# Kernel tuning notes

Measured on AMD Instinct MI355X. Metric: run time of the kernel, lower is better.

Reference implementation:

```python
import jax, jax.numpy as jnp
import numpy as np

E, N, NB = 250000, 20000, 8
D_EDGE, D_RBF, D_CBF, D_TRI = 128, 16, 16, 64
INV_SQRT_2 = 1.0 / np.sqrt(2.0).astype(np.float32)
INV_SQRT_NB = 1.0 / np.sqrt(float(NB))


def setup_inputs() -> dict:
    key = jax.random.key(0)
    ks = jax.random.split(key, 13)
    def w(k, fi, fo):
        return (jax.random.normal(k, (fi, fo), dtype=jnp.float32) / np.sqrt(fi)).astype(jnp.float32)
    return {
        "m_st": jax.random.normal(ks[0], (E, D_EDGE), dtype=jnp.float32),
        "rbf": jax.random.normal(ks[1], (E, D_RBF), dtype=jnp.float32),
        "cbf": jax.random.normal(ks[2], (E, NB, D_CBF), dtype=jnp.float32),
        "idx_s": jax.random.randint(ks[3], (E,), 0, N),
        "idx_swap": jax.random.randint(ks[4], (E,), 0, E),
        "basis_idx1": jax.random.randint(ks[5], (N, NB), 0, E),
        "W_m_rbf": w(ks[6], D_EDGE, D_EDGE),
        "W_rbf": w(ks[7], D_RBF, D_EDGE),
        "W_m_cbf": w(ks[8], D_EDGE, D_TRI),
        "W_cbf": w(ks[9], D_CBF, D_TRI),
        "W_dir": w(ks[10], D_TRI, D_EDGE),
        "W_st": w(ks[11], D_EDGE, D_EDGE),
        "W_ts": w(ks[12], D_EDGE, D_EDGE),
    }


def reference(m_st, rbf, cbf, idx_s, idx_swap, basis_idx1,
              W_m_rbf, W_rbf, W_m_cbf, W_cbf, W_dir, W_st, W_ts):
    act = jax.nn.silu
    # gather per-edge basis indices: (E, NB) -> (E*NB,)
    b1 = basis_idx1[idx_s].reshape(-1)
    # rbf branch (ScaleFactor == 1.0 at init -> identity)
    m = act(m_st @ W_m_rbf)                     # (E, D_EDGE)
    m = m * (rbf @ W_rbf)                       # (E, D_EDGE)
    # cbf branch
    e, nb, c = cbf.shape
    cbf2 = cbf.reshape(e * nb, c)               # (E*NB, D_CBF)
    m_nb = act(m @ W_m_cbf)                     # (E, D_TRI)
    m_nb = m_nb[b1]                             # gather -> (E*NB, D_TRI)
    m_nb = m_nb * (cbf2 @ W_cbf)                # (E*NB, D_TRI)
    x = m_nb.reshape(e, nb, -1).sum(1) * INV_SQRT_NB  # (E, D_TRI)
    x = act(x @ W_dir)                          # (E, D_EDGE)
    x_st = act(x @ W_st)
    x_ts = act(x @ W_ts)[idx_swap]              # swap-gather
    return (x_st + x_ts) * INV_SQRT_2
```

## Files before the change

kernel.cpp:

```cpp
#include <hip/hip_runtime.h>


#define DEV __device__ __forceinline__

typedef __attribute__((ext_vector_type(8))) short bf16x8;
typedef __attribute__((ext_vector_type(4))) float f32x4;

constexpr int E = 250000;
constexpr float INV_SQRT_2  = 0.70710678118654752f;
constexpr float INV_SQRT_NB = 0.35355339059327373f;

constexpr int PW1 = 0;
constexpr int PW2 = 16384;
constexpr int PW3 = 20480;
constexpr int PWD = 28672;
constexpr int PWS = 36864;
constexpr int PWT = 53248;
constexpr int PWC = 69632;
constexpr int PACK_TOTAL = 72192;

constexpr size_t OFF_T = 1u << 18;
constexpr size_t OFF_Z = OFF_T + (size_t)E * 64 * 2;
constexpr size_t WS_NEED_FAST = OFF_Z + (size_t)E * 128 * 4;

DEV unsigned short f2bf(float f) {
  __bf16 h = (__bf16)f;
  unsigned short u;
  __builtin_memcpy(&u, &h, 2);
  return u;
}
DEV unsigned f2bfpk(float lo, float hi) {
  return (unsigned)f2bf(lo) | ((unsigned)f2bf(hi) << 16);
}
DEV float bf2f(unsigned short h) { return __uint_as_float((unsigned)h << 16); }
DEV float silu_f(float x) { return x / (1.f + __expf(-x)); }

__global__ __launch_bounds__(256) void k0_pack(
    const float* __restrict__ W1, const float* __restrict__ W2,
    const float* __restrict__ W3, const float* __restrict__ Wc,
    const float* __restrict__ Wd, const float* __restrict__ Ws,
    const float* __restrict__ Wt, unsigned short* __restrict__ pack) {
  int idx = blockIdx.x * 256 + threadIdx.x;
  if (idx >= PACK_TOTAL) return;
  float v = 0.f;
  if (idx < PW2)      { int i = idx;       int n = i >> 7, k = i & 127; v = W1[k * 128 + n]; }
  else if (idx < PW3) { int i = idx - PW2; int n = i >> 5, k = i & 31;  v = (k < 16) ? W2[k * 128 + n] : 0.f; }
  else if (idx < PWD) { int i = idx - PW3; int n = i >> 7, k = i & 127; v = W3[k * 64 + n]; }
  else if (idx < PWS) { int i = idx - PWD; int n = i >> 6, k = i & 63;  v = Wd[k * 128 + n]; }
  else if (idx < PWT) { int i = idx - PWS; int n = i >> 7, k = i & 127; v = Ws[k * 128 + n]; }
  else if (idx < PWC) { int i = idx - PWT; int n = i >> 7, k = i & 127; v = Wt[k * 128 + n]; }
  else                { int i = idx - PWC; int n = i / 40, k = i % 40;  v = (k < 16) ? Wc[k * 64 + n] : 0.f; }
  pack[idx] = f2bf(v);
}

__global__ __launch_bounds__(512) void k1_mbranch(
    const float* __restrict__ m_st, const float* __restrict__ rbf,
    const unsigned short* __restrict__ pack, unsigned short* __restrict__ tT) {
  __shared__ __align__(16) unsigned short sA[128 * 136];
  __shared__ __align__(16) unsigned short sR[128 * 40];
  const int tid = threadIdx.x;
  const int e0 = blockIdx.x * 128;

  #pragma unroll
  for (int it = 0; it < 8; ++it) {
    int i = tid + it * 512;
    int row = i >> 5, kh = i & 31;
    int er = min(e0 + row, E - 1);
    const float4 v = *(const float4*)(m_st + (size_t)er * 128 + kh * 4);
    uint2 o;
    o.x = f2bfpk(v.x, v.y); o.y = f2bfpk(v.z, v.w);
    *(uint2*)(sA + row * 136 + kh * 4) = o;
  }
  {
    int row = tid >> 2, kh = tid & 3;
    int er = min(e0 + row, E - 1);
    const float4 v = *(const float4*)(rbf + (size_t)er * 16 + kh * 4);
    uint2 o;
    o.x = f2bfpk(v.x, v.y); o.y = f2bfpk(v.z, v.w);
    *(uint2*)(sR + row * 40 + kh * 4) = o;
    uint2 zz = {0u, 0u};
    *(uint2*)(sR + row * 40 + 16 + kh * 4) = zz;
  }
  __syncthreads();

  const int lane = tid & 63, wv = tid >> 6;
  const int m = lane & 15, q = lane >> 4;
  const int arow = wv * 16 + m;

  const f32x4 zero4 = {0.f, 0.f, 0.f, 0.f};
  f32x4 macc[8], racc[8];
  #pragma unroll
  for (int nt = 0; nt < 8; ++nt) { macc[nt] = zero4; racc[nt] = zero4; }

  {
    bf16x8 a = *(const bf16x8*)(sR + arow * 40 + q * 8);
    #pragma unroll
    for (int nt = 0; nt < 8; ++nt) {
      bf16x8 b = *(const bf16x8*)(pack + PW2 + (nt * 16 + m) * 32 + q * 8);
      racc[nt] = __builtin_amdgcn_mfma_f32_16x16x32_bf16(a, b, racc[nt], 0, 0, 0);
    }
  }
  #pragma unroll
  for (int kk = 0; kk < 4; ++kk) {
    bf16x8 a = *(const bf16x8*)(sA + arow * 136 + kk * 32 + q * 8);
    #pragma unroll
    for (int nt = 0; nt < 8; ++nt) {
      bf16x8 b = *(const bf16x8*)(pack + PW1 + (nt * 16 + m) * 128 + kk * 32 + q * 8);
      macc[nt] = __builtin_amdgcn_mfma_f32_16x16x32_bf16(a, b, macc[nt], 0, 0, 0);
    }
  }
  #pragma unroll
  for (int nt = 0; nt < 8; ++nt)
    #pragma unroll
    for (int r = 0; r < 4; ++r) {
      float v = silu_f(macc[nt][r]) * racc[nt][r];
      sA[(wv * 16 + q * 4 + r) * 136 + nt * 16 + m] = f2bf(v);
    }
  __syncthreads();

  f32x4 tacc[4];
  #pragma unroll
  for (int nt = 0; nt < 4; ++nt) tacc[nt] = zero4;
  #pragma unroll
  for (int kk = 0; kk < 4; ++kk) {
    bf16x8 a = *(const bf16x8*)(sA + arow * 136 + kk * 32 + q * 8);
    #pragma unroll
    for (int nt = 0; nt < 4; ++nt) {
      bf16x8 b = *(const bf16x8*)(pack + PW3 + (nt * 16 + m) * 128 + kk * 32 + q * 8);
      tacc[nt] = __builtin_amdgcn_mfma_f32_16x16x32_bf16(a, b, tacc[nt], 0, 0, 0);
    }
  }
  #pragma unroll
  for (int r = 0; r < 4; ++r) {
    int erow = e0 + wv * 16 + q * 4 + r;
    if (erow < E) {
      uint2 o;
      o.x = f2bfpk(silu_f(tacc[0][r]), silu_f(tacc[1][r]));
      o.y = f2bfpk(silu_f(tacc[2][r]), silu_f(tacc[3][r]));
      *(uint2*)(tT + (size_t)erow * 64 + m * 4) = o;
    }
  }
}

DEV bf16x8 cbf_pack8(const float4& c0, const float4& c1) {
  unsigned u[4];
  u[0] = f2bfpk(c0.x, c0.y);
  u[1] = f2bfpk(c0.z, c0.w);
  u[2] = f2bfpk(c1.x, c1.y);
  u[3] = f2bfpk(c1.z, c1.w);
  bf16x8 r;
  __builtin_memcpy(&r, u, 16);
  return r;
}

DEV void x_issue(const float* __restrict__ cbf, const int* sB,
                 const unsigned short* __restrict__ tT,
                 int wv, int m, int q, int mt, long long rowA, long long rowB,
                 float4& c0, float4& c1, ushort4* tv) {
  if (q < 2) {
    long long row = (m < 8) ? rowA + m : rowB + (m - 8);
    c0 = *(const float4*)(cbf + row * 16 + q * 8);
    c1 = *(const float4*)(cbf + row * 16 + q * 8 + 4);
  }
  const int lrb = wv * 128 + mt * 16 + q * 4;
  #pragma unroll
  for (int r = 0; r < 4; ++r) {
    int brow = sB[lrb + r];
    tv[r] = *(const ushort4*)(tT + (size_t)brow * 64 + m * 4);
  }
}

DEV void x_compute(const bf16x8* bw, unsigned short* sX,
                   int wv, int m, int q, int mt,
                   const float4& c0, const float4& c1,
                   const ushort4& tv0, const ushort4& tv1,
                   const ushort4& tv2, const ushort4& tv3) {
  bf16x8 af = {0, 0, 0, 0, 0, 0, 0, 0};
  if (q < 2) af = cbf_pack8(c0, c1);
  const f32x4 zero4 = {0.f, 0.f, 0.f, 0.f};
  f32x4 p0 = zero4, p1 = zero4, p2 = zero4, p3 = zero4;
  p0 = __builtin_amdgcn_mfma_f32_16x16x32_bf16(af, bw[0], p0, 0, 0, 0);
  p1 = __builtin_amdgcn_mfma_f32_16x16x32_bf16(af, bw[1], p1, 0, 0, 0);
  p2 = __builtin_amdgcn_mfma_f32_16x16x32_bf16(af, bw[2], p2, 0, 0, 0);
  p3 = __builtin_amdgcn_mfma_f32_16x16x32_bf16(af, bw[3], p3, 0, 0, 0);

  float s0 = bf2f(tv0.x) * p0[0] + bf2f(tv1.x) * p0[1] + bf2f(tv2.x) * p0[2] + bf2f(tv3.x) * p0[3];
  float s1 = bf2f(tv0.y) * p1[0] + bf2f(tv1.y) * p1[1] + bf2f(tv2.y) * p1[2] + bf2f(tv3.y) * p1[3];
  float s2 = bf2f(tv0.z) * p2[0] + bf2f(tv1.z) * p2[1] + bf2f(tv2.z) * p2[2] + bf2f(tv3.z) * p2[3];
  float s3 = bf2f(tv0.w) * p3[0] + bf2f(tv1.w) * p3[1] + bf2f(tv2.w) * p3[2] + bf2f(tv3.w) * p3[3];

  s0 += __shfl_xor(s0, 16);
  s1 += __shfl_xor(s1, 16);
  s2 += __shfl_xor(s2, 16);
  s3 += __shfl_xor(s3, 16);

  int lrow = wv * 16 + mt * 2 + (q >> 1);
  if (q == 0 || q == 2) {
    sX[lrow * 72 +  0 + m] = f2bf(s0 * INV_SQRT_NB);
    sX[lrow * 72 + 16 + m] = f2bf(s1 * INV_SQRT_NB);
    sX[lrow * 72 + 32 + m] = f2bf(s2 * INV_SQRT_NB);
    sX[lrow * 72 + 48 + m] = f2bf(s3 * INV_SQRT_NB);
  }
}

DEV void xtile_gather_reduce(
    const float* __restrict__ cbf, const int* sB,
    const unsigned short* __restrict__ tT, const bf16x8* bw,
    unsigned short* sX,
    int wv, int m, int q, long long rowA, long long rowB, int mt) {
  float4 c0, c1;
  ushort4 tv[4];
  x_issue(cbf, sB, tT, wv, m, q, mt, rowA, rowB, c0, c1, tv);
  x_compute(bw, sX, wv, m, q, mt, c0, c1, tv[0], tv[1], tv[2], tv[3]);
}

DEV void ytile(const unsigned short* __restrict__ pack,
               const unsigned short* sX,
               unsigned short* sY, int wv, int m, int q) {
  const int arow = wv * 16 + m;
  const f32x4 zero4 = {0.f, 0.f, 0.f, 0.f};
  f32x4 yacc[8];
  #pragma unroll
  for (int nt = 0; nt < 8; ++nt) yacc[nt] = zero4;
  #pragma unroll
  for (int kk = 0; kk < 2; ++kk) {
    bf16x8 a = *(const bf16x8*)(sX + arow * 72 + kk * 32 + q * 8);
    #pragma unroll
    for (int nt = 0; nt < 8; ++nt) {
      bf16x8 b = *(const bf16x8*)(pack + PWD + (nt * 16 + m) * 64 + kk * 32 + q * 8);
      yacc[nt] = __builtin_amdgcn_mfma_f32_16x16x32_bf16(a, b, yacc[nt], 0, 0, 0);
    }
  }
  #pragma unroll
  for (int nt = 0; nt < 8; ++nt)
    #pragma unroll
    for (int r = 0; r < 4; ++r)
      sY[(wv * 16 + q * 4 + r) * 136 + nt * 16 + m] = f2bf(silu_f(yacc[nt][r]));
}

__global__ __launch_bounds__(512) void k2_fused(
    const float* __restrict__ cbf, const int* __restrict__ idx_s,
    const int* __restrict__ basis_idx1, const unsigned short* __restrict__ pack,
    const unsigned short* __restrict__ tT, float* __restrict__ out,
    float* __restrict__ zbuf) {
  __shared__ __align__(16) unsigned char sU[34816];
  __shared__ __align__(16) unsigned short sX[128 * 72];
  unsigned short* sWc = (unsigned short*)sU;
  int* sB1 = (int*)(sU + 5120);
  unsigned short* sY = (unsigned short*)sU;
  const int tid = threadIdx.x;
  const int e0 = blockIdx.x * 128;

  ((uint2*)sWc)[tid] = ((const uint2*)(pack + PWC))[tid];
  if (tid < 128) ((uint2*)sWc)[512 + tid] = ((const uint2*)(pack + PWC))[512 + tid];
  #pragma unroll
  for (int it = 0; it < 2; ++it) {
    int i = tid + it * 512;
    int e = min(e0 + (i >> 3), E - 1);
    int b = basis_idx1[idx_s[e] * 8 + (i & 7)];
    sB1[i] = min(max(b, 0), E - 1);
  }
  __syncthreads();

  const int lane = tid & 63, wv = tid >> 6;
  const int m = lane & 15, q = lane >> 4;

  bf16x8 bw[4];
  #pragma unroll
  for (int nt = 0; nt < 4; ++nt)
    bw[nt] = *(const bf16x8*)(sWc + (nt * 16 + m) * 40 + q * 8);

  float4 pc0[2], pc1[2];
  ushort4 ptv[2][4];
  {
    int ea = min(e0 + wv * 16, E - 1), eb = min(ea + 1, E - 1);
    x_issue(cbf, sB1, tT, wv, m, q, 0, (long long)ea * 8, (long long)eb * 8,
            pc0[0], pc1[0], ptv[0]);
    ea = min(e0 + wv * 16 + 2, E - 1); eb = min(ea + 1, E - 1);
    x_issue(cbf, sB1, tT, wv, m, q, 1, (long long)ea * 8, (long long)eb * 8,
            pc0[1], pc1[1], ptv[1]);
  }
  #pragma unroll
  for (int mt = 0; mt < 8; ++mt) {
    const int s = mt & 1;
    float4 c0 = pc0[s], c1 = pc1[s];
    ushort4 tv0 = ptv[s][0], tv1 = ptv[s][1], tv2 = ptv[s][2], tv3 = ptv[s][3];
    if (mt + 2 < 8) {
      int ea = min(e0 + wv * 16 + (mt + 2) * 2, E - 1), eb = min(ea + 1, E - 1);
      x_issue(cbf, sB1, tT, wv, m, q, mt + 2, (long long)ea * 8, (long long)eb * 8,
              pc0[s], pc1[s], ptv[s]);
    }
    x_compute(bw, sX, wv, m, q, mt, c0, c1, tv0, tv1, tv2, tv3);
  }
  __syncthreads();

  ytile(pack, sX, sY, wv, m, q);
  __syncthreads();

  const int arow = wv * 16 + m;
  const f32x4 zero4 = {0.f, 0.f, 0.f, 0.f};
  f32x4 acc[8];
  #pragma unroll
  for (int nt = 0; nt < 8; ++nt) acc[nt] = zero4;
  #pragma unroll
  for (int kk = 0; kk < 4; ++kk) {
    bf16x8 a = *(const bf16x8*)(sY + arow * 136 + kk * 32 + q * 8);
    #pragma unroll
    for (int nt = 0; nt < 8; ++nt) {
      bf16x8 b = *(const bf16x8*)(pack + PWS + (nt * 16 + m) * 128 + kk * 32 + q * 8);
      acc[nt] = __builtin_amdgcn_mfma_f32_16x16x32_bf16(a, b, acc[nt], 0, 0, 0);
    }
  }
  #pragma unroll
  for (int nt = 0; nt < 8; ++nt)
    #pragma unroll
    for (int r = 0; r < 4; ++r) {
      int erow = e0 + wv * 16 + q * 4 + r;
      if (erow < E) out[(size_t)erow * 128 + nt * 16 + m] = silu_f(acc[nt][r]);
    }

  if (zbuf) {
    #pragma unroll
    for (int nt = 0; nt < 8; ++nt) acc[nt] = zero4;
    #pragma unroll
    for (int kk = 0; kk < 4; ++kk) {
      bf16x8 a = *(const bf16x8*)(sY + arow * 136 + kk * 32 + q * 8);
      #pragma unroll
      for (int nt = 0; nt < 8; ++nt) {
        bf16x8 b = *(const bf16x8*)(pack + PWT + (nt * 16 + m) * 128 + kk * 32 + q * 8);
        acc[nt] = __builtin_amdgcn_mfma_f32_16x16x32_bf16(a, b, acc[nt], 0, 0, 0);
      }
    }
    #pragma unroll
    for (int nt = 0; nt < 8; ++nt)
      #pragma unroll
      for (int r = 0; r < 4; ++r) {
        int erow = e0 + wv * 16 + q * 4 + r;
        if (erow < E) zbuf[(size_t)erow * 128 + nt * 16 + m] = silu_f(acc[nt][r]);
      }
  }
}

__global__ __launch_bounds__(256) void k3_combine(
    const int* __restrict__ idx_swap, const float* __restrict__ zbuf,
    float* __restrict__ out) {
  int t = blockIdx.x * 256 + threadIdx.x;
  int e = t >> 5, c = t & 31;
  if (e >= E) return;
  int f = idx_swap[e];
  f = min(max(f, 0), E - 1);
  float4 o = ((const float4*)out)[t];
  float4 z = ((const float4*)zbuf)[(size_t)f * 32 + c];
  o.x = (o.x + z.x) * INV_SQRT_2;
  o.y = (o.y + z.y) * INV_SQRT_2;
  o.z = (o.z + z.z) * INV_SQRT_2;
  o.w = (o.w + z.w) * INV_SQRT_2;
  ((float4*)out)[t] = o;
}

__global__ __launch_bounds__(512) void k3_swap(
    const float* __restrict__ cbf, const int* __restrict__ idx_s,
    const int* __restrict__ idx_swap, const int* __restrict__ basis_idx1,
    const unsigned short* __restrict__ pack, const unsigned short* __restrict__ tT,
    float* __restrict__ out) {
  __shared__ __align__(16) unsigned short sWc[64 * 40];
  __shared__ int sSE[128];
  __shared__ int sB3[1024];
  __shared__ __align__(16) unsigned short sX[128 * 72];
  __shared__ __align__(16) unsigned short sY[128 * 136];
  const int tid = threadIdx.x;
  const int e0 = blockIdx.x * 128;

  ((uint2*)sWc)[tid] = ((const uint2*)(pack + PWC))[tid];
  if (tid < 128) {
    ((uint2*)sWc)[512 + tid] = ((const uint2*)(pack + PWC))[512 + tid];
    int f = idx_swap[min(e0 + tid, E - 1)];
    sSE[tid] = min(max(f, 0), E - 1);
  }
  __syncthreads();
  #pragma unroll
  for (int it = 0; it < 2; ++it) {
    int i = tid + it * 512;
    int f = sSE[i >> 3];
    int b = basis_idx1[idx_s[f] * 8 + (i & 7)];
    sB3[i] = min(max(b, 0), E - 1);
  }
  __syncthreads();

  const int lane = tid & 63, wv = tid >> 6;
  const int m = lane & 15, q = lane >> 4;

  bf16x8 bw[4];
  #pragma unroll
  for (int nt = 0; nt < 4; ++nt)
    bw[nt] = *(const bf16x8*)(sWc + (nt * 16 + m) * 40 + q * 8);

  for (int mt = 0; mt < 8; ++mt) {
    int le = wv * 16 + mt * 2;
    long long fa = sSE[le], fb = sSE[le + 1];
    xtile_gather_reduce(cbf, sB3, tT, bw, sX, wv, m, q, fa * 8, fb * 8, mt);
  }
  __syncthreads();

  ytile(pack, sX, sY, wv, m, q);
  __syncthreads();

  const int arow = wv * 16 + m;
  const f32x4 zero4 = {0.f, 0.f, 0.f, 0.f};
  f32x4 acc[8];
  #pragma unroll
  for (int nt = 0; nt < 8; ++nt) acc[nt] = zero4;
  #pragma unroll
  for (int kk = 0; kk < 4; ++kk) {
    bf16x8 a = *(const bf16x8*)(sY + arow * 136 + kk * 32 + q * 8);
    #pragma unroll
    for (int nt = 0; nt < 8; ++nt) {
      bf16x8 b = *(const bf16x8*)(pack + PWT + (nt * 16 + m) * 128 + kk * 32 + q * 8);
      acc[nt] = __builtin_amdgcn_mfma_f32_16x16x32_bf16(a, b, acc[nt], 0, 0, 0);
    }
  }
  #pragma unroll
  for (int nt = 0; nt < 8; ++nt)
    #pragma unroll
    for (int r = 0; r < 4; ++r) {
      int erow = e0 + wv * 16 + q * 4 + r;
      if (erow < E) {
        size_t o = (size_t)erow * 128 + nt * 16 + m;
        out[o] = (out[o] + silu_f(acc[nt][r])) * INV_SQRT_2;
      }
    }
}

extern "C" void kernel_launch(void* const* d_in, const int* in_sizes, int n_in,
                              void* d_out, int out_size, void* d_ws, size_t ws_size,
                              hipStream_t stream) {
  const float* m_st = (const float*)d_in[0];
  const float* rbf  = (const float*)d_in[1];
  const float* cbf  = (const float*)d_in[2];
  const int* idx_s  = (const int*)d_in[3];
  const int* idx_sw = (const int*)d_in[4];
  const int* bidx   = (const int*)d_in[5];
  const float* W1 = (const float*)d_in[6];
  const float* W2 = (const float*)d_in[7];
  const float* W3 = (const float*)d_in[8];
  const float* Wc = (const float*)d_in[9];
  const float* Wd = (const float*)d_in[10];
  const float* Ws = (const float*)d_in[11];
  const float* Wt = (const float*)d_in[12];

  unsigned short* pack = (unsigned short*)d_ws;
  unsigned short* tT   = (unsigned short*)((char*)d_ws + OFF_T);
  float* zbuf = (ws_size >= WS_NEED_FAST) ? (float*)((char*)d_ws + OFF_Z) : nullptr;
  float* out = (float*)d_out;

  const int nb = (E + 127) / 128;
  k0_pack<<<(PACK_TOTAL + 255) / 256, 256, 0, stream>>>(W1, W2, W3, Wc, Wd, Ws, Wt, pack);
  k1_mbranch<<<nb, 512, 0, stream>>>(m_st, rbf, pack, tT);
  k2_fused<<<nb, 512, 0, stream>>>(cbf, idx_s, bidx, pack, tT, out, zbuf);
  if (zbuf) {
    k3_combine<<<(E * 32 + 255) / 256, 256, 0, stream>>>(idx_sw, zbuf, out);
  } else {
    k3_swap<<<nb, 512, 0, stream>>>(cbf, idx_s, idx_sw, bidx, pack, tT, out);
  }
}
```

Before: 639.5 us.

## Split fused cbf gather kernel into gather pass and GEMM pass via workspace

```diff
diff --git a/kernel.cpp b/kernel.cpp
--- a/kernel.cpp
+++ b/kernel.cpp
@@ -22,6 +22,8 @@
 constexpr size_t OFF_T = 1u << 18;
 constexpr size_t OFF_Z = OFF_T + (size_t)E * 64 * 2;
 constexpr size_t WS_NEED_FAST = OFF_Z + (size_t)E * 128 * 4;
+constexpr size_t OFF_X = WS_NEED_FAST;
+constexpr size_t WS_NEED_SPLIT = OFF_X + (size_t)E * 64 * 2;
 
 DEV unsigned short f2bf(float f) {
   __bf16 h = (__bf16)f;
@@ -238,6 +240,149 @@
       sY[(wv * 16 + q * 4 + r) * 136 + nt * 16 + m] = f2bf(silu_f(yacc[nt][r]));
 }
 
+__global__ __launch_bounds__(512) void k2a_gather(
+    const float* __restrict__ cbf, const int* __restrict__ idx_s,
+    const int* __restrict__ basis_idx1, const unsigned short* __restrict__ pack,
+    const unsigned short* __restrict__ tT, unsigned short* __restrict__ xbuf) {
+  __shared__ __align__(16) unsigned short sWc[64 * 40];
+  __shared__ int sB1[1024];
+  const int tid = threadIdx.x;
+  const int e0 = blockIdx.x * 128;
+
+  ((uint2*)sWc)[tid] = ((const uint2*)(pack + PWC))[tid];
+  if (tid < 128) ((uint2*)sWc)[512 + tid] = ((const uint2*)(pack + PWC))[512 + tid];
+  #pragma unroll
+  for (int it = 0; it < 2; ++it) {
+    int i = tid + it * 512;
+    int e = min(e0 + (i >> 3), E - 1);
+    int b = basis_idx1[idx_s[e] * 8 + (i & 7)];
+    sB1[i] = min(max(b, 0), E - 1);
+  }
+  __syncthreads();
+
+  const int lane = tid & 63, wv = tid >> 6;
+  const int m = lane & 15, q = lane >> 4;
+
+  bf16x8 bw[4];
+  #pragma unroll
+  for (int nt = 0; nt < 4; ++nt)
+    bw[nt] = *(const bf16x8*)(sWc + (nt * 16 + m) * 40 + q * 8);
+
+  const f32x4 zero4 = {0.f, 0.f, 0.f, 0.f};
+  #pragma unroll
+  for (int mt = 0; mt < 8; ++mt) {
+    int ea = min(e0 + wv * 16 + mt * 2, E - 1), eb = min(ea + 1, E - 1);
+    bf16x8 af = {0, 0, 0, 0, 0, 0, 0, 0};
+    if (q < 2) {
+      long long row = (long long)((m < 8) ? ea : eb) * 8 + (m & 7);
+      float4 c0 = *(const float4*)(cbf + row * 16 + q * 8);
+      float4 c1 = *(const float4*)(cbf + row * 16 + q * 8 + 4);
+      af = cbf_pack8(c0, c1);
+    }
+    f32x4 p0 = __builtin_amdgcn_mfma_f32_16x16x32_bf16(af, bw[0], zero4, 0, 0, 0);
+    f32x4 p1 = __builtin_amdgcn_mfma_f32_16x16x32_bf16(af, bw[1], zero4, 0, 0, 0);
+    f32x4 p2 = __builtin_amdgcn_mfma_f32_16x16x32_bf16(af, bw[2], zero4, 0, 0, 0);
+    f32x4 p3 = __builtin_amdgcn_mfma_f32_16x16x32_bf16(af, bw[3], zero4, 0, 0, 0);
+
+    const int lrb = wv * 128 + mt * 16 + q * 4;
+    float s0 = 0.f, s1 = 0.f, s2 = 0.f, s3 = 0.f;
+    #pragma unroll
+    for (int r = 0; r < 4; ++r) {
+      int brow = sB1[lrb + r];
+      ushort4 tv = *(const ushort4*)(tT + (size_t)brow * 64 + m * 4);
+      s0 += bf2f(tv.x) * p0[r];
+      s1 += bf2f(tv.y) * p1[r];
+      s2 += bf2f(tv.z) * p2[r];
+      s3 += bf2f(tv.w) * p3[r];
+    }
+    s0 += __shfl_xor(s0, 16);
+    s1 += __shfl_xor(s1, 16);
+    s2 += __shfl_xor(s2, 16);
+    s3 += __shfl_xor(s3, 16);
+
+    if (q == 0 || q == 2) {
+      int erow = e0 + wv * 16 + mt * 2 + (q >> 1);
+      if (erow < E) {
+        ushort4 o;
+        o.x = f2bf(s0 * INV_SQRT_NB);
+        o.y = f2bf(s1 * INV_SQRT_NB);
+        o.z = f2bf(s2 * INV_SQRT_NB);
+        o.w = f2bf(s3 * INV_SQRT_NB);
+        *(ushort4*)(xbuf + (size_t)erow * 64 + m * 4) = o;
+      }
+    }
+  }
+}
+
+__global__ __launch_bounds__(512) void k2b_gemm(
+    const unsigned short* __restrict__ pack, const unsigned short* __restrict__ xbuf,
+    float* __restrict__ out, float* __restrict__ zbuf) {
+  __shared__ __align__(16) unsigned short sX[128 * 72];
+  __shared__ __align__(16) unsigned short sY[128 * 136];
+  const int tid = threadIdx.x;
+  const int e0 = blockIdx.x * 128;
+
+  #pragma unroll
+  for (int it = 0; it < 4; ++it) {
+    int i = tid + it * 512;
+    int row = i >> 4, mm = i & 15;
+    int er = min(e0 + row, E - 1);
+    ushort4 v = *(const ushort4*)(xbuf + (size_t)er * 64 + mm * 4);
+    sX[row * 72 +  0 + mm] = v.x;
+    sX[row * 72 + 16 + mm] = v.y;
+    sX[row * 72 + 32 + mm] = v.z;
+    sX[row * 72 + 48 + mm] = v.w;
+  }
+  __syncthreads();
+
+  const int lane = tid & 63, wv = tid >> 6;
+  const int m = lane & 15, q = lane >> 4;
+
+  ytile(pack, sX, sY, wv, m, q);
+  __syncthreads();
+
+  const int arow = wv * 16 + m;
+  const f32x4 zero4 = {0.f, 0.f, 0.f, 0.f};
+  f32x4 acc[8];
+  #pragma unroll
+  for (int nt = 0; nt < 8; ++nt) acc[nt] = zero4;
+  #pragma unroll
+  for (int kk = 0; kk < 4; ++kk) {
+    bf16x8 a = *(const bf16x8*)(sY + arow * 136 + kk * 32 + q * 8);
+    #pragma unroll
+    for (int nt = 0; nt < 8; ++nt) {
+      bf16x8 b = *(const bf16x8*)(pack + PWS + (nt * 16 + m) * 128 + kk * 32 + q * 8);
+      acc[nt] = __builtin_amdgcn_mfma_f32_16x16x32_bf16(a, b, acc[nt], 0, 0, 0);
+    }
+  }
+  #pragma unroll
+  for (int nt = 0; nt < 8; ++nt)
+    #pragma unroll
+    for (int r = 0; r < 4; ++r) {
+      int erow = e0 + wv * 16 + q * 4 + r;
+      if (erow < E) out[(size_t)erow * 128 + nt * 16 + m] = silu_f(acc[nt][r]);
+    }
+
+  #pragma unroll
+  for (int nt = 0; nt < 8; ++nt) acc[nt] = zero4;
+  #pragma unroll
+  for (int kk = 0; kk < 4; ++kk) {
+    bf16x8 a = *(const bf16x8*)(sY + arow * 136 + kk * 32 + q * 8);
+    #pragma unroll
+    for (int nt = 0; nt < 8; ++nt) {
+      bf16x8 b = *(const bf16x8*)(pack + PWT + (nt * 16 + m) * 128 + kk * 32 + q * 8);
+      acc[nt] = __builtin_amdgcn_mfma_f32_16x16x32_bf16(a, b, acc[nt], 0, 0, 0);
+    }
+  }
+  #pragma unroll
+  for (int nt = 0; nt < 8; ++nt)
+    #pragma unroll
+    for (int r = 0; r < 4; ++r) {
+      int erow = e0 + wv * 16 + q * 4 + r;
+      if (erow < E) zbuf[(size_t)erow * 128 + nt * 16 + m] = silu_f(acc[nt][r]);
+    }
+}
+
 __global__ __launch_bounds__(512) void k2_fused(
     const float* __restrict__ cbf, const int* __restrict__ idx_s,
     const int* __restrict__ basis_idx1, const unsigned short* __restrict__ pack,
@@ -270,27 +415,10 @@
   for (int nt = 0; nt < 4; ++nt)
     bw[nt] = *(const bf16x8*)(sWc + (nt * 16 + m) * 40 + q * 8);
 
-  float4 pc0[2], pc1[2];
-  ushort4 ptv[2][4];
-  {
-    int ea = min(e0 + wv * 16, E - 1), eb = min(ea + 1, E - 1);
-    x_issue(cbf, sB1, tT, wv, m, q, 0, (long long)ea * 8, (long long)eb * 8,
-            pc0[0], pc1[0], ptv[0]);
-    ea = min(e0 + wv * 16 + 2, E - 1); eb = min(ea + 1, E - 1);
-    x_issue(cbf, sB1, tT, wv, m, q, 1, (long long)ea * 8, (long long)eb * 8,
-            pc0[1], pc1[1], ptv[1]);
-  }
-  #pragma unroll
   for (int mt = 0; mt < 8; ++mt) {
-    const int s = mt & 1;
-    float4 c0 = pc0[s], c1 = pc1[s];
-    ushort4 tv0 = ptv[s][0], tv1 = ptv[s][1], tv2 = ptv[s][2], tv3 = ptv[s][3];
-    if (mt + 2 < 8) {
-      int ea = min(e0 + wv * 16 + (mt + 2) * 2, E - 1), eb = min(ea + 1, E - 1);
-      x_issue(cbf, sB1, tT, wv, m, q, mt + 2, (long long)ea * 8, (long long)eb * 8,
-              pc0[s], pc1[s], ptv[s]);
-    }
-    x_compute(bw, sX, wv, m, q, mt, c0, c1, tv0, tv1, tv2, tv3);
+    int ea = min(e0 + wv * 16 + mt * 2, E - 1), eb = min(ea + 1, E - 1);
+    xtile_gather_reduce(cbf, sB1, tT, bw, sX, wv, m, q,
+                        (long long)ea * 8, (long long)eb * 8, mt);
   }
   __syncthreads();
 
@@ -451,15 +579,21 @@
   unsigned short* pack = (unsigned short*)d_ws;
   unsigned short* tT   = (unsigned short*)((char*)d_ws + OFF_T);
   float* zbuf = (ws_size >= WS_NEED_FAST) ? (float*)((char*)d_ws + OFF_Z) : nullptr;
+  unsigned short* xbuf = (ws_size >= WS_NEED_SPLIT) ? (unsigned short*)((char*)d_ws + OFF_X) : nullptr;
   float* out = (float*)d_out;
 
   const int nb = (E + 127) / 128;
   k0_pack<<<(PACK_TOTAL + 255) / 256, 256, 0, stream>>>(W1, W2, W3, Wc, Wd, Ws, Wt, pack);
   k1_mbranch<<<nb, 512, 0, stream>>>(m_st, rbf, pack, tT);
-  k2_fused<<<nb, 512, 0, stream>>>(cbf, idx_s, bidx, pack, tT, out, zbuf);
-  if (zbuf) {
+  if (zbuf && xbuf) {
+    k2a_gather<<<nb, 512, 0, stream>>>(cbf, idx_s, bidx, pack, tT, xbuf);
+    k2b_gemm<<<nb, 512, 0, stream>>>(pack, xbuf, out, zbuf);
+    k3_combine<<<(E * 32 + 255) / 256, 256, 0, stream>>>(idx_sw, zbuf, out);
+  } else if (zbuf) {
+    k2_fused<<<nb, 512, 0, stream>>>(cbf, idx_s, bidx, pack, tT, out, zbuf);
     k3_combine<<<(E * 32 + 255) / 256, 256, 0, stream>>>(idx_sw, zbuf, out);
   } else {
+    k2_fused<<<nb, 512, 0, stream>>>(cbf, idx_s, bidx, pack, tT, out, nullptr);
     k3_swap<<<nb, 512, 0, stream>>>(cbf, idx_s, idx_sw, bidx, pack, tT, out);
   }
 }
```

Result: no change. 643.3 us (+0.6%).
